# Kernel tuning notes

Measured on AMD Instinct MI355X. Metric: run time of the kernel, lower is better.

The kernel has to match this reference:

```python
import math
import jax, jax.numpy as jnp
import numpy as np
from jax import lax

B, T, D, H = 4, 1024, 1024, 8192
EPS = 1e-6
PLIF_TH = 0.05        # plif_threshold init
SURR_ALPHA = 2.0      # atan surrogate sharpness
SPARSITY = 0.95

@jax.custom_vjp
def spike(v):
    # Heaviside forward, atan surrogate backward (spikingjelly-style)
    return (v > 0).astype(v.dtype)

def _spike_fwd(v):
    return (v > 0).astype(v.dtype), v

def _spike_bwd(v, g):
    return (g * (SURR_ALPHA / 2.0) / (1.0 + (math.pi / 2.0 * SURR_ALPHA * v) ** 2),)

spike.defvjp(_spike_fwd, _spike_bwd)

def rmsnorm(x, w):
    return x * lax.rsqrt(jnp.mean(x * x, axis=-1, keepdims=True) + EPS) * w

def setup_inputs() -> dict:
    key = jax.random.key(0)
    ks = jax.random.split(key, 12)
    std = 0.02
    return {
        "x": jax.random.normal(ks[0], (B, T, D), jnp.float32),
        "ln1_w": jnp.ones((D,), jnp.float32),
        "liq_Wi": jax.random.normal(ks[1], (D, D), jnp.float32) * std,
        "liq_Wr": jax.random.normal(ks[2], (D, D), jnp.float32) * std,
        "liq_b": jnp.zeros((D,), jnp.float32),
        "liq_tau": 0.5 + jax.random.uniform(ks[3], (D,), jnp.float32),  # positive time constants ('hasani' init)
        "plif_tau": jnp.full((1,), 2.5, jnp.float32),                   # plif_tau_init=2.5
        "syn_w": jax.random.normal(ks[4], (D, D), jnp.float32) * std,
        "gate_w": jax.random.normal(ks[5], (D, D), jnp.float32) * 0.01,
        "gate_b": jnp.zeros((D,), jnp.float32),
        "ln2_w": jnp.ones((D,), jnp.float32),
        "ffn_wg": jax.random.normal(ks[6], (H, D), jnp.float32) * std,
        "ffn_wu": jax.random.normal(ks[7], (H, D), jnp.float32) * std,
        "ffn_wd": jax.random.normal(ks[8], (D, H), jnp.float32) * (std / math.sqrt(2.0)),
        "syn_mask": jax.random.uniform(ks[9], (D, D), jnp.float32) < (1.0 - SPARSITY),
    }

def _forward(x, ln1_w, liq_Wi, liq_Wr, liq_b, liq_tau, plif_tau,
             syn_w, gate_w, gate_b, ln2_w, ffn_wg, ffn_wu, ffn_wd, syn_mask):
    a = rmsnorm(x, ln1_w)                                   # (B,T,D)
    # LiquidCell: ODE-style leaky recurrence, h_t = h*e^{-1/tau} + (1-e^{-1/tau})*tanh(Wi x + Wr h + b)
    decay = jnp.exp(-1.0 / liq_tau)                         # (D,)
    def liq_step(h, xt):
        f = jnp.tanh(xt @ liq_Wi.T + h @ liq_Wr.T + liq_b)
        h2 = h * decay + (1.0 - decay) * f
        return h2, h2
    _, hs = lax.scan(liq_step, jnp.zeros((B, D), x.dtype), jnp.swapaxes(a, 0, 1))
    h = jnp.swapaxes(hs, 0, 1)                              # (B,T,D)
    # PLIFCell.forward_seq: v += (h_t - v)/tau; spike; subtract reset
    inv_tau = 1.0 / plif_tau[0]
    def plif_step(v, ht):
        v = v + (ht - v) * inv_tau
        s = spike(v - PLIF_TH)
        return v - s * PLIF_TH, s
    _, ss = lax.scan(plif_step, jnp.zeros((B, D), x.dtype), jnp.swapaxes(h, 0, 1))
    s = jnp.swapaxes(ss, 0, 1)                              # (B,T,D) binary spikes
    w_eff = syn_w * syn_mask.astype(syn_w.dtype)
    syn_out = s @ w_eff.T
    gated = syn_out * jax.nn.sigmoid(s @ gate_w.T + gate_b)
    x = x + gated
    y = rmsnorm(x, ln2_w)
    ffn = (jax.nn.silu(y @ ffn_wg.T) * (y @ ffn_wu.T)) @ ffn_wd.T
    return x + ffn

def reference(x, ln1_w, liq_Wi, liq_Wr, liq_b, liq_tau, plif_tau,
              syn_w, gate_w, gate_b, ln2_w, ffn_wg, ffn_wu, ffn_wd, syn_mask):
    return _forward(x, ln1_w, liq_Wi, liq_Wr, liq_b, liq_tau, plif_tau,
                    syn_w, gate_w, gate_b, ln2_w, ffn_wg, ffn_wu, ffn_wd, syn_mask)
```

## Files before the change

kernel.cpp:

```cpp
#include <hip/hip_runtime.h>
#include <math.h>


#define Bsz 4
#define Tsz 1024
#define Dsz 1024
#define Hsz 8192

typedef __attribute__((ext_vector_type(8))) short short8;
typedef __attribute__((ext_vector_type(4))) float floatx4_t;


__device__ __forceinline__ unsigned short f2bf(float f) {
  union { float f; unsigned u; } c; c.f = f;
  unsigned x = c.u;
  unsigned r = (x + 0x7FFFu + ((x >> 16) & 1u)) >> 16;
  return (unsigned short)r;
}

__device__ __forceinline__ void gll16(const void* gsrc, void* ldst) {
  __builtin_amdgcn_global_load_lds(
      (const __attribute__((address_space(1))) unsigned int*)gsrc,
      (__attribute__((address_space(3))) unsigned int*)ldst,
      16, 0, 0);
}


__global__ void zero_u64_k(unsigned long long* p, int n) {
  int i = blockIdx.x * 256 + threadIdx.x;
  if (i < n) p[i] = 0ull;
}

__global__ void detect_mask_k(const unsigned int* m, int* mode) {
  if (blockIdx.x == 0 && threadIdx.x == 0) {
    int md = 0;
    for (int i = 0; i < 256; ++i) {
      unsigned w = m[i];
      if (w == 0x3F800000u) { md = 2; break; }
      if (w > 1u) md = 1;
    }
    *mode = md;
  }
}

__global__ void cvt_bf16_k(const float* __restrict__ in,
                           unsigned short* __restrict__ out, int n4) {
  int i = blockIdx.x * 256 + threadIdx.x;
  if (i < n4) {
    float4 v = ((const float4*)in)[i];
    ushort4 o;
    o.x = f2bf(v.x); o.y = f2bf(v.y); o.z = f2bf(v.z); o.w = f2bf(v.w);
    ((ushort4*)out)[i] = o;
  }
}

__global__ void make_weff_k(const float* __restrict__ syn,
                            const void* __restrict__ mask,
                            const int* __restrict__ mode,
                            unsigned short* __restrict__ out, int n) {
  int i = blockIdx.x * 256 + threadIdx.x;
  if (i < n) {
    int md = *mode;
    bool on;
    if (md == 1)      on = ((const unsigned char*)mask)[i] != 0;
    else if (md == 2) on = ((const float*)mask)[i] != 0.f;
    else              on = ((const int*)mask)[i] != 0;
    out[i] = on ? f2bf(syn[i]) : (unsigned short)0;
  }
}


template<int BF16OUT>
__global__ __launch_bounds__(256)
void rmsnorm_k(const float* __restrict__ X, const float* __restrict__ w,
               void* __restrict__ out) {
  const long row = blockIdx.x;
  const float* x = X + row * Dsz;
  float4 v = ((const float4*)x)[threadIdx.x];
  float ss = v.x * v.x + v.y * v.y + v.z * v.z + v.w * v.w;
#pragma unroll
  for (int off = 32; off > 0; off >>= 1) ss += __shfl_down(ss, off);
  __shared__ float red[4];
  if ((threadIdx.x & 63) == 0) red[threadIdx.x >> 6] = ss;
  __syncthreads();
  float tot = red[0] + red[1] + red[2] + red[3];
  float scale = 1.0f / sqrtf(tot * (1.0f / Dsz) + 1e-6f);
  float4 wv = ((const float4*)w)[threadIdx.x];
  float o0 = v.x * scale * wv.x, o1 = v.y * scale * wv.y;
  float o2 = v.z * scale * wv.z, o3 = v.w * scale * wv.w;
  if (BF16OUT) {
    ushort4 o; o.x = f2bf(o0); o.y = f2bf(o1); o.z = f2bf(o2); o.w = f2bf(o3);
    ((ushort4*)out)[row * 256 + threadIdx.x] = o;
  } else {
    float4 o; o.x = o0; o.y = o1; o.z = o2; o.w = o3;
    ((float4*)out)[row * 256 + threadIdx.x] = o;
  }
}


__global__ __launch_bounds__(256)
void gemm_f32_bt(const float* __restrict__ A, const float* __restrict__ Bm,
                 const float* __restrict__ bias, float* __restrict__ C,
                 int M, int N, int K) {
  __shared__ float sA[16][128 + 4];
  __shared__ float sB[16][64 + 4];
  const int bm = blockIdx.x, bn = blockIdx.y;
  const int tid = threadIdx.x;
  const int tx = tid & 15, ty = tid >> 4;
  float cacc[8][4] = {};
  for (int k0 = 0; k0 < K; k0 += 16) {
#pragma unroll
    for (int i = 0; i < 2; ++i) {
      int slot = tid * 2 + i, row = slot >> 2, kq = slot & 3;
      float4 v = *(const float4*)(A + (long)(bm * 128 + row) * K + k0 + kq * 4);
      sA[kq * 4 + 0][row] = v.x; sA[kq * 4 + 1][row] = v.y;
      sA[kq * 4 + 2][row] = v.z; sA[kq * 4 + 3][row] = v.w;
    }
    {
      int row = tid >> 2, kq = tid & 3;
      float4 v = *(const float4*)(Bm + (long)(bn * 64 + row) * K + k0 + kq * 4);
      sB[kq * 4 + 0][row] = v.x; sB[kq * 4 + 1][row] = v.y;
      sB[kq * 4 + 2][row] = v.z; sB[kq * 4 + 3][row] = v.w;
    }
    __syncthreads();
#pragma unroll
    for (int kk = 0; kk < 16; ++kk) {
      float4 A0 = *(const float4*)&sA[kk][ty * 8];
      float4 A1 = *(const float4*)&sA[kk][ty * 8 + 4];
      float4 B0 = *(const float4*)&sB[kk][tx * 4];
      float av[8] = {A0.x, A0.y, A0.z, A0.w, A1.x, A1.y, A1.z, A1.w};
      float bv[4] = {B0.x, B0.y, B0.z, B0.w};
#pragma unroll
      for (int r = 0; r < 8; ++r)
#pragma unroll
        for (int c = 0; c < 4; ++c) cacc[r][c] += av[r] * bv[c];
    }
    __syncthreads();
  }
#pragma unroll
  for (int r = 0; r < 8; ++r) {
#pragma unroll
    for (int c = 0; c < 4; ++c) {
      int col = bn * 64 + tx * 4 + c;
      C[(long)(bm * 128 + ty * 8 + r) * N + col] = cacc[r][c] + bias[col];
    }
  }
}


__global__ __launch_bounds__(320)
void liquid_plif_k(const float* __restrict__ Wr, const float* __restrict__ U,
                   const float* __restrict__ liq_tau,
                   const float* __restrict__ plif_tau,
                   unsigned long long* __restrict__ Hex,
                   unsigned short* __restrict__ Sout) {
  const int blk = blockIdx.x;
  const int b = blk >> 5;
  const int base = (blk & 31) * 32;
  const int tid = threadIdx.x;

  __shared__ float h_lds[1024];
  __shared__ __align__(16) float red[2][4][8][4];
  __shared__ int flags[2][4];

  if (tid < 8) ((int*)flags)[tid] = 0;
  __syncthreads();

  if (tid < 256) {
    const int l = tid & 63, w = tid >> 6;
    const int rg = tid & 7;
    const int ck = tid >> 3;
    const int win = 256 * w;

    float4 wr[4][8];
#pragma unroll
    for (int r = 0; r < 4; ++r) {
      const float* wrow = Wr + (long)(base + rg * 4 + r) * Dsz + ck * 32;
#pragma unroll
      for (int qq = 0; qq < 8; ++qq) {
        int q = (qq + ck) & 7;
        wr[r][qq] = *(const float4*)(wrow + q * 4);
      }
    }

    for (int t = 1; t <= Tsz; ++t) {
      const unsigned want = (unsigned)(t - 1);
      const unsigned long long* src =
          Hex + (((long)((t - 1) & 1) * Bsz + b) << 10) + win;
      unsigned long long a0, a1, a2, a3;
      for (;;) {
        a0 = __hip_atomic_load(src + l,       __ATOMIC_RELAXED, __HIP_MEMORY_SCOPE_AGENT);
        a1 = __hip_atomic_load(src + l + 64,  __ATOMIC_RELAXED, __HIP_MEMORY_SCOPE_AGENT);
        a2 = __hip_atomic_load(src + l + 128, __ATOMIC_RELAXED, __HIP_MEMORY_SCOPE_AGENT);
        a3 = __hip_atomic_load(src + l + 192, __ATOMIC_RELAXED, __HIP_MEMORY_SCOPE_AGENT);
        int ok = ((unsigned)(a0 >> 32) == want) & ((unsigned)(a1 >> 32) == want) &
                 ((unsigned)(a2 >> 32) == want) & ((unsigned)(a3 >> 32) == want);
        if (__all(ok)) break;
      }
      h_lds[win + l]       = __uint_as_float((unsigned)a0);
      h_lds[win + l + 64]  = __uint_as_float((unsigned)a1);
      h_lds[win + l + 128] = __uint_as_float((unsigned)a2);
      h_lds[win + l + 192] = __uint_as_float((unsigned)a3);

      float acc0 = 0.f, acc1 = 0.f, acc2 = 0.f, acc3 = 0.f;
      const float* hch = &h_lds[ck * 32];
#pragma unroll
      for (int qq = 0; qq < 8; ++qq) {
        const int q = (qq + ck) & 7;
        float4 hv = *(const float4*)(hch + q * 4);
        acc0 += wr[0][qq].x * hv.x + wr[0][qq].y * hv.y + wr[0][qq].z * hv.z + wr[0][qq].w * hv.w;
        acc1 += wr[1][qq].x * hv.x + wr[1][qq].y * hv.y + wr[1][qq].z * hv.z + wr[1][qq].w * hv.w;
        acc2 += wr[2][qq].x * hv.x + wr[2][qq].y * hv.y + wr[2][qq].z * hv.z + wr[2][qq].w * hv.w;
        acc3 += wr[3][qq].x * hv.x + wr[3][qq].y * hv.y + wr[3][qq].z * hv.z + wr[3][qq].w * hv.w;
      }
      acc0 += __shfl_xor(acc0, 8); acc0 += __shfl_xor(acc0, 16); acc0 += __shfl_xor(acc0, 32);
      acc1 += __shfl_xor(acc1, 8); acc1 += __shfl_xor(acc1, 16); acc1 += __shfl_xor(acc1, 32);
      acc2 += __shfl_xor(acc2, 8); acc2 += __shfl_xor(acc2, 16); acc2 += __shfl_xor(acc2, 32);
      acc3 += __shfl_xor(acc3, 8); acc3 += __shfl_xor(acc3, 16); acc3 += __shfl_xor(acc3, 32);
      if ((l & 56) == 0) {
        float4 rv; rv.x = acc0; rv.y = acc1; rv.z = acc2; rv.w = acc3;
        *(float4*)&red[t & 1][w][rg][0] = rv;
      }
      asm volatile("s_waitcnt lgkmcnt(0)" ::: "memory");
      if (l == 0)
        __hip_atomic_store(&flags[t & 1][w], t, __ATOMIC_RELEASE,
                           __HIP_MEMORY_SCOPE_WORKGROUP);
    }
  } else {
    const int r = tid - 256;
    float hstate = 0.f, vstate = 0.f, dec = 0.f, omdec = 0.f, itau = 0.f;
    if (r < 32) {
      float tau = liq_tau[base + r];
      dec = expf(-1.0f / tau);
      omdec = 1.0f - dec;
      itau = 1.0f / plif_tau[0];
    }
    for (int t = 1; t <= Tsz; ++t) {
      float uval = 0.f;
      if (r < 32)
        uval = U[((long)b * Tsz + (t - 1)) * Dsz + base + r];
      const int p = t & 1;
      for (;;) {
        int f0 = __hip_atomic_load(&flags[p][0], __ATOMIC_ACQUIRE, __HIP_MEMORY_SCOPE_WORKGROUP);
        int f1 = __hip_atomic_load(&flags[p][1], __ATOMIC_ACQUIRE, __HIP_MEMORY_SCOPE_WORKGROUP);
        int f2 = __hip_atomic_load(&flags[p][2], __ATOMIC_ACQUIRE, __HIP_MEMORY_SCOPE_WORKGROUP);
        int f3 = __hip_atomic_load(&flags[p][3], __ATOMIC_ACQUIRE, __HIP_MEMORY_SCOPE_WORKGROUP);
        if ((f0 == t) & (f1 == t) & (f2 == t) & (f3 == t)) break;
      }
      if (r < 32) {
        const int r2 = r >> 2, jj = r & 3;
        float sum = red[p][0][r2][jj] + red[p][1][r2][jj] +
                    red[p][2][r2][jj] + red[p][3][r2][jj];
        float z = sum + uval;
        float ex = __expf(2.0f * z);
        float f = 1.0f - 2.0f * __builtin_amdgcn_rcpf(ex + 1.0f);
        hstate = hstate * dec + omdec * f;
        vstate += (hstate - vstate) * itau;
        float sp = ((vstate - 0.05f) > 0.f) ? 1.f : 0.f;
        vstate -= sp * 0.05f;
        const long pidx = (((long)(t & 1) * Bsz + b) << 10) + base + r;
        unsigned long long pv =
            (((unsigned long long)(unsigned)t) << 32) |
            (unsigned long long)__float_as_uint(hstate);
        __hip_atomic_store(&Hex[pidx], pv, __ATOMIC_RELAXED,
                           __HIP_MEMORY_SCOPE_AGENT);
        Sout[((long)b * Tsz + (t - 1)) * Dsz + base + r] =
            (sp > 0.f) ? (unsigned short)0x3F80 : (unsigned short)0;
      }
    }
  }
}


template<int NB, int EPI>
__global__ __launch_bounds__(256)
void gemm_bt(const unsigned short* __restrict__ A,
             const unsigned short* __restrict__ B0,
             const unsigned short* __restrict__ B1,
             const float* __restrict__ aux0, const float* __restrict__ aux1,
             void* __restrict__ outp, int M, int N, int K) {
  __shared__ unsigned short sA[128 * 32];
  __shared__ unsigned short sB[2 * 128 * 32];
  const int tid = threadIdx.x;
  const int w = tid >> 6, l = tid & 63;
  const int wm = w & 1, wn = w >> 1;
  const int bm = blockIdx.x, bn = blockIdx.y;

  floatx4_t acc[NB][4][4];
#pragma unroll
  for (int j = 0; j < NB; ++j)
#pragma unroll
    for (int m = 0; m < 4; ++m)
#pragma unroll
      for (int n = 0; n < 4; ++n) acc[j][m][n] = (floatx4_t)(0.f);

  const int rA = bm * 128 + 16 * w + (l >> 2);
  const int rB = bn * 128 + 16 * w + (l >> 2);
  const int kl = (l & 3) * 8;
  const unsigned short* gA = A + (long)rA * K + kl;
  const unsigned short* gB0 = B0 + (long)rB * K + kl;
  const unsigned short* gB1 = nullptr;
  if constexpr (NB > 1) gB1 = B1 + (long)rB * K + kl;
  unsigned short* lA = &sA[(16 * w) * 32];
  unsigned short* lB = &sB[(16 * w) * 32];

  for (int k0 = 0; k0 < K; k0 += 32) {
    gll16(gA + k0,              lA);
    gll16(gA + k0 + 64 * K,     lA + 64 * 32);
    gll16(gB0 + k0,             lB);
    gll16(gB0 + k0 + 64 * K,    lB + 64 * 32);
    if constexpr (NB > 1) {
      gll16(gB1 + k0,           lB + 128 * 32);
      gll16(gB1 + k0 + 64 * K,  lB + 192 * 32);
    }
    __syncthreads();
    short8 af[4];
#pragma unroll
    for (int m = 0; m < 4; ++m)
      af[m] = *(const short8*)&sA[(wm * 64 + m * 16 + (l & 15)) * 32 + (l >> 4) * 8];
#pragma unroll
    for (int j = 0; j < NB; ++j) {
#pragma unroll
      for (int n = 0; n < 4; ++n) {
        short8 bf = *(const short8*)&sB[j * 128 * 32 +
                        (wn * 64 + n * 16 + (l & 15)) * 32 + (l >> 4) * 8];
#pragma unroll
        for (int m = 0; m < 4; ++m)
          acc[j][m][n] = __builtin_amdgcn_mfma_f32_16x16x32_bf16(
              af[m], bf, acc[j][m][n], 0, 0, 0);
      }
    }
    __syncthreads();
  }

  const int colBase = bn * 128 + wn * 64;
  const int rowBase = bm * 128 + wm * 64;
#pragma unroll
  for (int m = 0; m < 4; ++m) {
#pragma unroll
    for (int n = 0; n < 4; ++n) {
      const int col = colBase + n * 16 + (l & 15);
#pragma unroll
      for (int j = 0; j < 4; ++j) {
        const int row = rowBase + m * 16 + (l >> 4) * 4 + j;
        const long idx = (long)row * N + col;
        float v0 = acc[0][m][n][j];
        if constexpr (EPI == 1) {
          float gsum = acc[NB - 1][m][n][j] + aux1[col];
          float sg = 1.f / (1.f + __expf(-gsum));
          ((float*)outp)[idx] = aux0[idx] + v0 * sg;
        } else if constexpr (EPI == 2) {
          float sil = v0 / (1.f + __expf(-v0));
          ((unsigned short*)outp)[idx] = f2bf(sil * acc[NB - 1][m][n][j]);
        } else {
          ((float*)outp)[idx] = aux0[idx] + v0;
        }
      }
    }
  }
}


extern "C" void kernel_launch(void* const* d_in, const int* in_sizes, int n_in,
                              void* d_out, int out_size, void* d_ws, size_t ws_size,
                              hipStream_t stream) {
  (void)in_sizes; (void)n_in; (void)out_size; (void)ws_size;

  const float* x        = (const float*)d_in[0];
  const float* ln1_w    = (const float*)d_in[1];
  const float* liq_Wi   = (const float*)d_in[2];
  const float* liq_Wr   = (const float*)d_in[3];
  const float* liq_b    = (const float*)d_in[4];
  const float* liq_tau  = (const float*)d_in[5];
  const float* plif_tau = (const float*)d_in[6];
  const float* syn_w    = (const float*)d_in[7];
  const float* gate_w   = (const float*)d_in[8];
  const float* gate_b   = (const float*)d_in[9];
  const float* ln2_w    = (const float*)d_in[10];
  const float* ffn_wg   = (const float*)d_in[11];
  const float* ffn_wu   = (const float*)d_in[12];
  const float* ffn_wd   = (const float*)d_in[13];
  const void*  mask     = d_in[14];

  char* ws = (char*)d_ws;
  const size_t MB = 1024ull * 1024ull;
  unsigned short* wg_bf   = (unsigned short*)(ws + 0 * MB);
  unsigned short* wu_bf   = (unsigned short*)(ws + 16 * MB);
  unsigned short* wd_bf   = (unsigned short*)(ws + 32 * MB);
  unsigned short* weff_bf = (unsigned short*)(ws + 48 * MB);
  unsigned short* gw_bf   = (unsigned short*)(ws + 50 * MB);
  float*          x2_f    = (float*)         (ws + 52 * MB);
  unsigned short* s_bf    = (unsigned short*)(ws + 68 * MB);
  unsigned short* y_bf    = (unsigned short*)(ws + 76 * MB);
  unsigned short* ff_bf   = (unsigned short*)(ws + 84 * MB);
  float*          a_f     = (float*)         (ws + 84 * MB);
  float*          u_f     = (float*)         (ws + 100 * MB);
  unsigned long long* hex = (unsigned long long*)(ws + 148 * MB);
  int*            mode    = (int*)(ws + 148 * MB + 65536);
  float*          out_f   = (float*)d_out;

  const int M = Bsz * Tsz;

  detect_mask_k<<<1, 64, 0, stream>>>((const unsigned int*)mask, mode);
  cvt_bf16_k<<<(Hsz * Dsz / 4) / 256, 256, 0, stream>>>(ffn_wg, wg_bf, Hsz * Dsz / 4);
  cvt_bf16_k<<<(Hsz * Dsz / 4) / 256, 256, 0, stream>>>(ffn_wu, wu_bf, Hsz * Dsz / 4);
  cvt_bf16_k<<<(Dsz * Hsz / 4) / 256, 256, 0, stream>>>(ffn_wd, wd_bf, Dsz * Hsz / 4);
  cvt_bf16_k<<<(Dsz * Dsz / 4) / 256, 256, 0, stream>>>(gate_w, gw_bf, Dsz * Dsz / 4);
  make_weff_k<<<(Dsz * Dsz) / 256, 256, 0, stream>>>(syn_w, mask, mode, weff_bf, Dsz * Dsz);
  zero_u64_k<<<32, 256, 0, stream>>>(hex, 2 * Bsz * Dsz);

  rmsnorm_k<0><<<M, 256, 0, stream>>>(x, ln1_w, a_f);

  gemm_f32_bt<<<dim3(M / 128, Dsz / 64), 256, 0, stream>>>(
      a_f, liq_Wi, liq_b, u_f, M, Dsz, Dsz);

  liquid_plif_k<<<128, 320, 0, stream>>>(liq_Wr, u_f, liq_tau, plif_tau, hex, s_bf);

  gemm_bt<2, 1><<<dim3(M / 128, Dsz / 128), 256, 0, stream>>>(
      s_bf, weff_bf, gw_bf, x, gate_b, x2_f, M, Dsz, Dsz);

  rmsnorm_k<1><<<M, 256, 0, stream>>>(x2_f, ln2_w, y_bf);

  gemm_bt<2, 2><<<dim3(M / 128, Hsz / 128), 256, 0, stream>>>(
      y_bf, wg_bf, wu_bf, nullptr, nullptr, ff_bf, M, Hsz, Dsz);

  gemm_bt<1, 3><<<dim3(M / 128, Dsz / 128), 256, 0, stream>>>(
      ff_bf, wd_bf, nullptr, x2_f, nullptr, out_f, M, Dsz, Hsz);
}
```

Baseline: 2.392 ms.

## Overlap input projection and weight conversion with the liquid recurrence

```diff
diff --git a/kernel.cpp b/kernel.cpp
--- a/kernel.cpp
+++ b/kernel.cpp
@@ -29,44 +29,6 @@
 __global__ void zero_u64_k(unsigned long long* p, int n) {
   int i = blockIdx.x * 256 + threadIdx.x;
   if (i < n) p[i] = 0ull;
-}
-
-__global__ void detect_mask_k(const unsigned int* m, int* mode) {
-  if (blockIdx.x == 0 && threadIdx.x == 0) {
-    int md = 0;
-    for (int i = 0; i < 256; ++i) {
-      unsigned w = m[i];
-      if (w == 0x3F800000u) { md = 2; break; }
-      if (w > 1u) md = 1;
-    }
-    *mode = md;
-  }
-}
-
-__global__ void cvt_bf16_k(const float* __restrict__ in,
-                           unsigned short* __restrict__ out, int n4) {
-  int i = blockIdx.x * 256 + threadIdx.x;
-  if (i < n4) {
-    float4 v = ((const float4*)in)[i];
-    ushort4 o;
-    o.x = f2bf(v.x); o.y = f2bf(v.y); o.z = f2bf(v.z); o.w = f2bf(v.w);
-    ((ushort4*)out)[i] = o;
-  }
-}
-
-__global__ void make_weff_k(const float* __restrict__ syn,
-                            const void* __restrict__ mask,
-                            const int* __restrict__ mode,
-                            unsigned short* __restrict__ out, int n) {
-  int i = blockIdx.x * 256 + threadIdx.x;
-  if (i < n) {
-    int md = *mode;
-    bool on;
-    if (md == 1)      on = ((const unsigned char*)mask)[i] != 0;
-    else if (md == 2) on = ((const float*)mask)[i] != 0.f;
-    else              on = ((const int*)mask)[i] != 0;
-    out[i] = on ? f2bf(syn[i]) : (unsigned short)0;
-  }
 }
 
 
@@ -98,175 +60,269 @@
 }
 
 
-__global__ __launch_bounds__(256)
-void gemm_f32_bt(const float* __restrict__ A, const float* __restrict__ Bm,
-                 const float* __restrict__ bias, float* __restrict__ C,
-                 int M, int N, int K) {
-  __shared__ float sA[16][128 + 4];
-  __shared__ float sB[16][64 + 4];
-  const int bm = blockIdx.x, bn = blockIdx.y;
-  const int tid = threadIdx.x;
-  const int tx = tid & 15, ty = tid >> 4;
-  float cacc[8][4] = {};
-  for (int k0 = 0; k0 < K; k0 += 16) {
-#pragma unroll
-    for (int i = 0; i < 2; ++i) {
-      int slot = tid * 2 + i, row = slot >> 2, kq = slot & 3;
-      float4 v = *(const float4*)(A + (long)(bm * 128 + row) * K + k0 + kq * 4);
-      sA[kq * 4 + 0][row] = v.x; sA[kq * 4 + 1][row] = v.y;
-      sA[kq * 4 + 2][row] = v.z; sA[kq * 4 + 3][row] = v.w;
-    }
-    {
-      int row = tid >> 2, kq = tid & 3;
-      float4 v = *(const float4*)(Bm + (long)(bn * 64 + row) * K + k0 + kq * 4);
-      sB[kq * 4 + 0][row] = v.x; sB[kq * 4 + 1][row] = v.y;
-      sB[kq * 4 + 2][row] = v.z; sB[kq * 4 + 3][row] = v.w;
-    }
-    __syncthreads();
-#pragma unroll
-    for (int kk = 0; kk < 16; ++kk) {
-      float4 A0 = *(const float4*)&sA[kk][ty * 8];
-      float4 A1 = *(const float4*)&sA[kk][ty * 8 + 4];
-      float4 B0 = *(const float4*)&sB[kk][tx * 4];
-      float av[8] = {A0.x, A0.y, A0.z, A0.w, A1.x, A1.y, A1.z, A1.w};
-      float bv[4] = {B0.x, B0.y, B0.z, B0.w};
-#pragma unroll
-      for (int r = 0; r < 8; ++r)
-#pragma unroll
-        for (int c = 0; c < 4; ++c) cacc[r][c] += av[r] * bv[c];
-    }
-    __syncthreads();
-  }
-#pragma unroll
-  for (int r = 0; r < 8; ++r) {
-#pragma unroll
-    for (int c = 0; c < 4; ++c) {
-      int col = bn * 64 + tx * 4 + c;
-      C[(long)(bm * 128 + ty * 8 + r) * N + col] = cacc[r][c] + bias[col];
-    }
-  }
-}
-
-
 __global__ __launch_bounds__(320)
-void liquid_plif_k(const float* __restrict__ Wr, const float* __restrict__ U,
+void liquid_plif_k(const float* __restrict__ x,
+                   const float* __restrict__ ln1_w,
+                   const float* __restrict__ Wi,
+                   const float* __restrict__ liq_b,
+                   const float* __restrict__ Wr,
                    const float* __restrict__ liq_tau,
                    const float* __restrict__ plif_tau,
                    unsigned long long* __restrict__ Hex,
-                   unsigned short* __restrict__ Sout) {
-  const int blk = blockIdx.x;
-  const int b = blk >> 5;
-  const int base = (blk & 31) * 32;
+                   unsigned long long* __restrict__ Utag,
+                   unsigned short* __restrict__ Sout,
+                   const float* __restrict__ ffn_wg, unsigned short* wg_bf,
+                   const float* __restrict__ ffn_wu, unsigned short* wu_bf,
+                   const float* __restrict__ ffn_wd, unsigned short* wd_bf,
+                   const float* __restrict__ gate_w, unsigned short* gw_bf,
+                   const float* __restrict__ syn_w,  const void* mask,
+                   unsigned short* weff_bf) {
   const int tid = threadIdx.x;
 
   __shared__ float h_lds[1024];
   __shared__ __align__(16) float red[2][4][8][4];
   __shared__ int flags[2][4];
+  __shared__ float red4w[4];
+  __shared__ int s_mode;
 
   if (tid < 8) ((int*)flags)[tid] = 0;
   __syncthreads();
 
-  if (tid < 256) {
+  if (blockIdx.x < 128) {
+    const int blk = blockIdx.x;
+    const int b = blk >> 5;
+    const int base = (blk & 31) * 32;
+
+    if (tid < 256) {
+      const int l = tid & 63, w = tid >> 6;
+      const int rg = tid & 7;
+      const int ck = tid >> 3;
+      const int win = 256 * w;
+
+      float4 wr[4][8];
+#pragma unroll
+      for (int r = 0; r < 4; ++r) {
+        const float* wrow = Wr + (long)(base + rg * 4 + r) * Dsz + ck * 32;
+#pragma unroll
+        for (int qq = 0; qq < 8; ++qq) {
+          int q = (qq + ck) & 7;
+          wr[r][qq] = *(const float4*)(wrow + q * 4);
+        }
+      }
+
+      for (int t = 1; t <= Tsz; ++t) {
+        const unsigned want = (unsigned)(t - 1);
+        const unsigned long long* src =
+            Hex + (((long)((t - 1) & 1) * Bsz + b) << 10) + win;
+        unsigned long long a0, a1, a2, a3;
+        for (;;) {
+          a0 = __hip_atomic_load(src + l,       __ATOMIC_RELAXED, __HIP_MEMORY_SCOPE_AGENT);
+          a1 = __hip_atomic_load(src + l + 64,  __ATOMIC_RELAXED, __HIP_MEMORY_SCOPE_AGENT);
+          a2 = __hip_atomic_load(src + l + 128, __ATOMIC_RELAXED, __HIP_MEMORY_SCOPE_AGENT);
+          a3 = __hip_atomic_load(src + l + 192, __ATOMIC_RELAXED, __HIP_MEMORY_SCOPE_AGENT);
+          int ok = ((unsigned)(a0 >> 32) == want) & ((unsigned)(a1 >> 32) == want) &
+                   ((unsigned)(a2 >> 32) == want) & ((unsigned)(a3 >> 32) == want);
+          if (__all(ok)) break;
+        }
+        h_lds[win + l]       = __uint_as_float((unsigned)a0);
+        h_lds[win + l + 64]  = __uint_as_float((unsigned)a1);
+        h_lds[win + l + 128] = __uint_as_float((unsigned)a2);
+        h_lds[win + l + 192] = __uint_as_float((unsigned)a3);
+
+        float acc0 = 0.f, acc1 = 0.f, acc2 = 0.f, acc3 = 0.f;
+        const float* hch = &h_lds[ck * 32];
+#pragma unroll
+        for (int qq = 0; qq < 8; ++qq) {
+          const int q = (qq + ck) & 7;
+          float4 hv = *(const float4*)(hch + q * 4);
+          acc0 += wr[0][qq].x * hv.x + wr[0][qq].y * hv.y + wr[0][qq].z * hv.z + wr[0][qq].w * hv.w;
+          acc1 += wr[1][qq].x * hv.x + wr[1][qq].y * hv.y + wr[1][qq].z * hv.z + wr[1][qq].w * hv.w;
+          acc2 += wr[2][qq].x * hv.x + wr[2][qq].y * hv.y + wr[2][qq].z * hv.z + wr[2][qq].w * hv.w;
+          acc3 += wr[3][qq].x * hv.x + wr[3][qq].y * hv.y + wr[3][qq].z * hv.z + wr[3][qq].w * hv.w;
+        }
+        acc0 += __shfl_xor(acc0, 8); acc0 += __shfl_xor(acc0, 16); acc0 += __shfl_xor(acc0, 32);
+        acc1 += __shfl_xor(acc1, 8); acc1 += __shfl_xor(acc1, 16); acc1 += __shfl_xor(acc1, 32);
+        acc2 += __shfl_xor(acc2, 8); acc2 += __shfl_xor(acc2, 16); acc2 += __shfl_xor(acc2, 32);
+        acc3 += __shfl_xor(acc3, 8); acc3 += __shfl_xor(acc3, 16); acc3 += __shfl_xor(acc3, 32);
+        if ((l & 56) == 0) {
+          float4 rv; rv.x = acc0; rv.y = acc1; rv.z = acc2; rv.w = acc3;
+          *(float4*)&red[t & 1][w][rg][0] = rv;
+        }
+        asm volatile("s_waitcnt lgkmcnt(0)" ::: "memory");
+        if (l == 0)
+          __hip_atomic_store(&flags[t & 1][w], t, __ATOMIC_RELEASE,
+                             __HIP_MEMORY_SCOPE_WORKGROUP);
+      }
+    } else {
+      const int r = tid - 256;
+      float hstate = 0.f, vstate = 0.f, dec = 0.f, omdec = 0.f, itau = 0.f;
+      if (r < 32) {
+        float tau = liq_tau[base + r];
+        dec = expf(-1.0f / tau);
+        omdec = 1.0f - dec;
+        itau = 1.0f / plif_tau[0];
+      }
+      for (int t = 1; t <= Tsz; ++t) {
+        float uval = 0.f;
+        if (r < 32) {
+          const unsigned long long* up =
+              Utag + ((long)b * Tsz + (t - 1)) * Dsz + base + r;
+          unsigned long long uv;
+          do {
+            uv = __hip_atomic_load(up, __ATOMIC_RELAXED, __HIP_MEMORY_SCOPE_AGENT);
+          } while ((unsigned)(uv >> 32) != (unsigned)t);
+          uval = __uint_as_float((unsigned)uv);
+        }
+        const int p = t & 1;
+        for (;;) {
+          int f0 = __hip_atomic_load(&flags[p][0], __ATOMIC_ACQUIRE, __HIP_MEMORY_SCOPE_WORKGROUP);
+          int f1 = __hip_atomic_load(&flags[p][1], __ATOMIC_ACQUIRE, __HIP_MEMORY_SCOPE_WORKGROUP);
+          int f2 = __hip_atomic_load(&flags[p][2], __ATOMIC_ACQUIRE, __HIP_MEMORY_SCOPE_WORKGROUP);
+          int f3 = __hip_atomic_load(&flags[p][3], __ATOMIC_ACQUIRE, __HIP_MEMORY_SCOPE_WORKGROUP);
+          if ((f0 == t) & (f1 == t) & (f2 == t) & (f3 == t)) break;
+        }
+        if (r < 32) {
+          const int r2 = r >> 2, jj = r & 3;
+          float sum = red[p][0][r2][jj] + red[p][1][r2][jj] +
+                      red[p][2][r2][jj] + red[p][3][r2][jj];
+          float z = sum + uval;
+          float ex = __expf(2.0f * z);
+          float f = 1.0f - 2.0f * __builtin_amdgcn_rcpf(ex + 1.0f);
+          hstate = hstate * dec + omdec * f;
+          vstate += (hstate - vstate) * itau;
+          float sp = ((vstate - 0.05f) > 0.f) ? 1.f : 0.f;
+          vstate -= sp * 0.05f;
+          const long pidx = (((long)p * Bsz + b) << 10) + base + r;
+          unsigned long long pv =
+              (((unsigned long long)(unsigned)t) << 32) |
+              (unsigned long long)__float_as_uint(hstate);
+          __hip_atomic_store(&Hex[pidx], pv, __ATOMIC_RELAXED,
+                             __HIP_MEMORY_SCOPE_AGENT);
+          Sout[((long)b * Tsz + (t - 1)) * Dsz + base + r] =
+              (sp > 0.f) ? (unsigned short)0x3F80 : (unsigned short)0;
+        }
+      }
+    }
+  } else {
+    const int blk2 = blockIdx.x - 128;
+    const int b = blk2 >> 5;
+    const int base = (blk2 & 31) * 32;
+
     const int l = tid & 63, w = tid >> 6;
     const int rg = tid & 7;
     const int ck = tid >> 3;
-    const int win = 256 * w;
-
-    float4 wr[4][8];
-#pragma unroll
-    for (int r = 0; r < 4; ++r) {
-      const float* wrow = Wr + (long)(base + rg * 4 + r) * Dsz + ck * 32;
-#pragma unroll
-      for (int qq = 0; qq < 8; ++qq) {
-        int q = (qq + ck) & 7;
-        wr[r][qq] = *(const float4*)(wrow + q * 4);
-      }
-    }
+    float4 wi[4][8];
+    if (tid < 256) {
+#pragma unroll
+      for (int r = 0; r < 4; ++r) {
+        const float* wrow = Wi + (long)(base + rg * 4 + r) * Dsz + ck * 32;
+#pragma unroll
+        for (int qq = 0; qq < 8; ++qq) {
+          int q = (qq + ck) & 7;
+          wi[r][qq] = *(const float4*)(wrow + q * 4);
+        }
+      }
+    }
+    float4 w4 = (tid < 256) ? ((const float4*)ln1_w)[tid] : float4{0, 0, 0, 0};
+    float lb = 0.f;
+    if (tid >= 256 && (tid - 256) < 32) lb = liq_b[base + (tid - 256)];
 
     for (int t = 1; t <= Tsz; ++t) {
-      const unsigned want = (unsigned)(t - 1);
-      const unsigned long long* src =
-          Hex + (((long)((t - 1) & 1) * Bsz + b) << 10) + win;
-      unsigned long long a0, a1, a2, a3;
-      for (;;) {
-        a0 = __hip_atomic_load(src + l,       __ATOMIC_RELAXED, __HIP_MEMORY_SCOPE_AGENT);
-        a1 = __hip_atomic_load(src + l + 64,  __ATOMIC_RELAXED, __HIP_MEMORY_SCOPE_AGENT);
-        a2 = __hip_atomic_load(src + l + 128, __ATOMIC_RELAXED, __HIP_MEMORY_SCOPE_AGENT);
-        a3 = __hip_atomic_load(src + l + 192, __ATOMIC_RELAXED, __HIP_MEMORY_SCOPE_AGENT);
-        int ok = ((unsigned)(a0 >> 32) == want) & ((unsigned)(a1 >> 32) == want) &
-                 ((unsigned)(a2 >> 32) == want) & ((unsigned)(a3 >> 32) == want);
-        if (__all(ok)) break;
-      }
-      h_lds[win + l]       = __uint_as_float((unsigned)a0);
-      h_lds[win + l + 64]  = __uint_as_float((unsigned)a1);
-      h_lds[win + l + 128] = __uint_as_float((unsigned)a2);
-      h_lds[win + l + 192] = __uint_as_float((unsigned)a3);
-
-      float acc0 = 0.f, acc1 = 0.f, acc2 = 0.f, acc3 = 0.f;
-      const float* hch = &h_lds[ck * 32];
-#pragma unroll
-      for (int qq = 0; qq < 8; ++qq) {
-        const int q = (qq + ck) & 7;
-        float4 hv = *(const float4*)(hch + q * 4);
-        acc0 += wr[0][qq].x * hv.x + wr[0][qq].y * hv.y + wr[0][qq].z * hv.z + wr[0][qq].w * hv.w;
-        acc1 += wr[1][qq].x * hv.x + wr[1][qq].y * hv.y + wr[1][qq].z * hv.z + wr[1][qq].w * hv.w;
-        acc2 += wr[2][qq].x * hv.x + wr[2][qq].y * hv.y + wr[2][qq].z * hv.z + wr[2][qq].w * hv.w;
-        acc3 += wr[3][qq].x * hv.x + wr[3][qq].y * hv.y + wr[3][qq].z * hv.z + wr[3][qq].w * hv.w;
-      }
-      acc0 += __shfl_xor(acc0, 8); acc0 += __shfl_xor(acc0, 16); acc0 += __shfl_xor(acc0, 32);
-      acc1 += __shfl_xor(acc1, 8); acc1 += __shfl_xor(acc1, 16); acc1 += __shfl_xor(acc1, 32);
-      acc2 += __shfl_xor(acc2, 8); acc2 += __shfl_xor(acc2, 16); acc2 += __shfl_xor(acc2, 32);
-      acc3 += __shfl_xor(acc3, 8); acc3 += __shfl_xor(acc3, 16); acc3 += __shfl_xor(acc3, 32);
-      if ((l & 56) == 0) {
-        float4 rv; rv.x = acc0; rv.y = acc1; rv.z = acc2; rv.w = acc3;
-        *(float4*)&red[t & 1][w][rg][0] = rv;
-      }
-      asm volatile("s_waitcnt lgkmcnt(0)" ::: "memory");
-      if (l == 0)
-        __hip_atomic_store(&flags[t & 1][w], t, __ATOMIC_RELEASE,
-                           __HIP_MEMORY_SCOPE_WORKGROUP);
-    }
-  } else {
-    const int r = tid - 256;
-    float hstate = 0.f, vstate = 0.f, dec = 0.f, omdec = 0.f, itau = 0.f;
-    if (r < 32) {
-      float tau = liq_tau[base + r];
-      dec = expf(-1.0f / tau);
-      omdec = 1.0f - dec;
-      itau = 1.0f / plif_tau[0];
-    }
-    for (int t = 1; t <= Tsz; ++t) {
-      float uval = 0.f;
-      if (r < 32)
-        uval = U[((long)b * Tsz + (t - 1)) * Dsz + base + r];
-      const int p = t & 1;
-      for (;;) {
-        int f0 = __hip_atomic_load(&flags[p][0], __ATOMIC_ACQUIRE, __HIP_MEMORY_SCOPE_WORKGROUP);
-        int f1 = __hip_atomic_load(&flags[p][1], __ATOMIC_ACQUIRE, __HIP_MEMORY_SCOPE_WORKGROUP);
-        int f2 = __hip_atomic_load(&flags[p][2], __ATOMIC_ACQUIRE, __HIP_MEMORY_SCOPE_WORKGROUP);
-        int f3 = __hip_atomic_load(&flags[p][3], __ATOMIC_ACQUIRE, __HIP_MEMORY_SCOPE_WORKGROUP);
-        if ((f0 == t) & (f1 == t) & (f2 == t) & (f3 == t)) break;
-      }
-      if (r < 32) {
-        const int r2 = r >> 2, jj = r & 3;
-        float sum = red[p][0][r2][jj] + red[p][1][r2][jj] +
-                    red[p][2][r2][jj] + red[p][3][r2][jj];
-        float z = sum + uval;
-        float ex = __expf(2.0f * z);
-        float f = 1.0f - 2.0f * __builtin_amdgcn_rcpf(ex + 1.0f);
-        hstate = hstate * dec + omdec * f;
-        vstate += (hstate - vstate) * itau;
-        float sp = ((vstate - 0.05f) > 0.f) ? 1.f : 0.f;
-        vstate -= sp * 0.05f;
-        const long pidx = (((long)(t & 1) * Bsz + b) << 10) + base + r;
-        unsigned long long pv =
-            (((unsigned long long)(unsigned)t) << 32) |
-            (unsigned long long)__float_as_uint(hstate);
-        __hip_atomic_store(&Hex[pidx], pv, __ATOMIC_RELAXED,
-                           __HIP_MEMORY_SCOPE_AGENT);
-        Sout[((long)b * Tsz + (t - 1)) * Dsz + base + r] =
-            (sp > 0.f) ? (unsigned short)0x3F80 : (unsigned short)0;
-      }
+      float4 xv = {0, 0, 0, 0};
+      if (tid < 256) {
+        xv = ((const float4*)(x + ((long)b * Tsz + (t - 1)) * Dsz))[tid];
+        float ss = xv.x * xv.x + xv.y * xv.y + xv.z * xv.z + xv.w * xv.w;
+#pragma unroll
+        for (int off = 32; off > 0; off >>= 1) ss += __shfl_down(ss, off);
+        if (l == 0) red4w[w] = ss;
+      }
+      __syncthreads();
+      if (tid < 256) {
+        float tot = red4w[0] + red4w[1] + red4w[2] + red4w[3];
+        float scale = 1.0f / sqrtf(tot * (1.0f / Dsz) + 1e-6f);
+        float4 av;
+        av.x = xv.x * scale * w4.x; av.y = xv.y * scale * w4.y;
+        av.z = xv.z * scale * w4.z; av.w = xv.w * scale * w4.w;
+        ((float4*)h_lds)[tid] = av;
+      }
+      __syncthreads();
+      if (tid < 256) {
+        float acc0 = 0.f, acc1 = 0.f, acc2 = 0.f, acc3 = 0.f;
+        const float* hch = &h_lds[ck * 32];
+#pragma unroll
+        for (int qq = 0; qq < 8; ++qq) {
+          const int q = (qq + ck) & 7;
+          float4 hv = *(const float4*)(hch + q * 4);
+          acc0 += wi[0][qq].x * hv.x + wi[0][qq].y * hv.y + wi[0][qq].z * hv.z + wi[0][qq].w * hv.w;
+          acc1 += wi[1][qq].x * hv.x + wi[1][qq].y * hv.y + wi[1][qq].z * hv.z + wi[1][qq].w * hv.w;
+          acc2 += wi[2][qq].x * hv.x + wi[2][qq].y * hv.y + wi[2][qq].z * hv.z + wi[2][qq].w * hv.w;
+          acc3 += wi[3][qq].x * hv.x + wi[3][qq].y * hv.y + wi[3][qq].z * hv.z + wi[3][qq].w * hv.w;
+        }
+        acc0 += __shfl_xor(acc0, 8); acc0 += __shfl_xor(acc0, 16); acc0 += __shfl_xor(acc0, 32);
+        acc1 += __shfl_xor(acc1, 8); acc1 += __shfl_xor(acc1, 16); acc1 += __shfl_xor(acc1, 32);
+        acc2 += __shfl_xor(acc2, 8); acc2 += __shfl_xor(acc2, 16); acc2 += __shfl_xor(acc2, 32);
+        acc3 += __shfl_xor(acc3, 8); acc3 += __shfl_xor(acc3, 16); acc3 += __shfl_xor(acc3, 32);
+        if ((l & 56) == 0) {
+          float4 rv; rv.x = acc0; rv.y = acc1; rv.z = acc2; rv.w = acc3;
+          *(float4*)&red[0][w][rg][0] = rv;
+        }
+      }
+      __syncthreads();
+      if (tid >= 256) {
+        const int r = tid - 256;
+        if (r < 32) {
+          const int r2 = r >> 2, jj = r & 3;
+          float sum = red[0][0][r2][jj] + red[0][1][r2][jj] +
+                      red[0][2][r2][jj] + red[0][3][r2][jj] + lb;
+          unsigned long long pv =
+              (((unsigned long long)(unsigned)t) << 32) |
+              (unsigned long long)__float_as_uint(sum);
+          __hip_atomic_store(&Utag[((long)b * Tsz + (t - 1)) * Dsz + base + r],
+                             pv, __ATOMIC_RELAXED, __HIP_MEMORY_SCOPE_AGENT);
+        }
+      }
+      __syncthreads();
+    }
+
+    if (tid == 0) {
+      int md = 0;
+      const unsigned* m = (const unsigned*)mask;
+      for (int i = 0; i < 256; ++i) {
+        unsigned wd = m[i];
+        if (wd == 0x3F800000u) { md = 2; break; }
+        if (wd > 1u) md = 1;
+      }
+      s_mode = md;
+    }
+    __syncthreads();
+    const int md = s_mode;
+    const long gtid = (long)blk2 * 320 + tid;
+    const long gstr = 128 * 320;
+    const int n4big = Hsz * Dsz / 4;
+    for (long i = gtid; i < n4big; i += gstr) {
+      float4 v = ((const float4*)ffn_wg)[i];
+      ushort4 o; o.x = f2bf(v.x); o.y = f2bf(v.y); o.z = f2bf(v.z); o.w = f2bf(v.w);
+      ((ushort4*)wg_bf)[i] = o;
+      v = ((const float4*)ffn_wu)[i];
+      o.x = f2bf(v.x); o.y = f2bf(v.y); o.z = f2bf(v.z); o.w = f2bf(v.w);
+      ((ushort4*)wu_bf)[i] = o;
+      v = ((const float4*)ffn_wd)[i];
+      o.x = f2bf(v.x); o.y = f2bf(v.y); o.z = f2bf(v.z); o.w = f2bf(v.w);
+      ((ushort4*)wd_bf)[i] = o;
+    }
+    const int n4g = Dsz * Dsz / 4;
+    for (long i = gtid; i < n4g; i += gstr) {
+      float4 v = ((const float4*)gate_w)[i];
+      ushort4 o; o.x = f2bf(v.x); o.y = f2bf(v.y); o.z = f2bf(v.z); o.w = f2bf(v.w);
+      ((ushort4*)gw_bf)[i] = o;
+    }
+    const int nw = Dsz * Dsz;
+    for (long i = gtid; i < nw; i += gstr) {
+      bool on;
+      if (md == 1)      on = ((const unsigned char*)mask)[i] != 0;
+      else if (md == 2) on = ((const float*)mask)[i] != 0.f;
+      else              on = ((const int*)mask)[i] != 0;
+      weff_bf[i] = on ? f2bf(syn_w[i]) : (unsigned short)0;
     }
   }
 }
@@ -393,28 +449,18 @@
   unsigned short* s_bf    = (unsigned short*)(ws + 68 * MB);
   unsigned short* y_bf    = (unsigned short*)(ws + 76 * MB);
   unsigned short* ff_bf   = (unsigned short*)(ws + 84 * MB);
-  float*          a_f     = (float*)         (ws + 84 * MB);
-  float*          u_f     = (float*)         (ws + 100 * MB);
+  unsigned long long* Utag= (unsigned long long*)(ws + 84 * MB);
   unsigned long long* hex = (unsigned long long*)(ws + 148 * MB);
-  int*            mode    = (int*)(ws + 148 * MB + 65536);
   float*          out_f   = (float*)d_out;
 
   const int M = Bsz * Tsz;
 
-  detect_mask_k<<<1, 64, 0, stream>>>((const unsigned int*)mask, mode);
-  cvt_bf16_k<<<(Hsz * Dsz / 4) / 256, 256, 0, stream>>>(ffn_wg, wg_bf, Hsz * Dsz / 4);
-  cvt_bf16_k<<<(Hsz * Dsz / 4) / 256, 256, 0, stream>>>(ffn_wu, wu_bf, Hsz * Dsz / 4);
-  cvt_bf16_k<<<(Dsz * Hsz / 4) / 256, 256, 0, stream>>>(ffn_wd, wd_bf, Dsz * Hsz / 4);
-  cvt_bf16_k<<<(Dsz * Dsz / 4) / 256, 256, 0, stream>>>(gate_w, gw_bf, Dsz * Dsz / 4);
-  make_weff_k<<<(Dsz * Dsz) / 256, 256, 0, stream>>>(syn_w, mask, mode, weff_bf, Dsz * Dsz);
   zero_u64_k<<<32, 256, 0, stream>>>(hex, 2 * Bsz * Dsz);
 
-  rmsnorm_k<0><<<M, 256, 0, stream>>>(x, ln1_w, a_f);
-
-  gemm_f32_bt<<<dim3(M / 128, Dsz / 64), 256, 0, stream>>>(
-      a_f, liq_Wi, liq_b, u_f, M, Dsz, Dsz);
-
-  liquid_plif_k<<<128, 320, 0, stream>>>(liq_Wr, u_f, liq_tau, plif_tau, hex, s_bf);
+  liquid_plif_k<<<256, 320, 0, stream>>>(
+      x, ln1_w, liq_Wi, liq_b, liq_Wr, liq_tau, plif_tau, hex, Utag, s_bf,
+      ffn_wg, wg_bf, ffn_wu, wu_bf, ffn_wd, wd_bf, gate_w, gw_bf,
+      syn_w, mask, weff_bf);
 
   gemm_bt<2, 1><<<dim3(M / 128, Dsz / 128), 256, 0, stream>>>(
       s_bf, weff_bf, gw_bf, x, gate_b, x2_f, M, Dsz, Dsz);
```

After: 2.213 ms. 7.5% less time.
